# Kernel optimization log

Measured on AMD Instinct MI355X. Metric: run time of the kernel, lower is better.

The kernel has to match this reference:

```python
import jax, jax.numpy as jnp
import numpy as np

N, E = 100000, 1600000
IN_C, OUT_C, H, EDGE_DIM = 128, 64, 2, 4
NEG_SLOPE = 0.2
LN_EPS = 1e-5


def setup_inputs() -> dict:
    key = jax.random.key(0)
    ks = jax.random.split(key, 12)
    s = 1.0 / np.sqrt(IN_C)
    inp = {
        "x": jax.random.normal(ks[0], (N, IN_C), jnp.float32),
        "edge_index": jax.random.randint(ks[1], (2, E), 0, N, jnp.int64),
        "edge_attr": jax.random.normal(ks[2], (E, EDGE_DIM), jnp.float32),
        "W": jax.random.normal(ks[3], (IN_C, H * OUT_C), jnp.float32) * s,
        "att_src": jax.random.normal(ks[4], (H, OUT_C), jnp.float32) * s,
        "att_dst": jax.random.normal(ks[5], (H, OUT_C), jnp.float32) * s,
        "W_edge": jax.random.normal(ks[6], (EDGE_DIM, H * OUT_C), jnp.float32) * 0.5,
        "att_edge": jax.random.normal(ks[7], (H, OUT_C), jnp.float32) * s,
        "bias": jnp.zeros((OUT_C,), jnp.float32),
        "gamma": jnp.ones((OUT_C,), jnp.float32),
        "beta": jnp.zeros((OUT_C,), jnp.float32),
    }
    return inp


def reference(x, edge_index, edge_attr, W, att_src, att_dst, W_edge, att_edge, bias, gamma, beta):
    n = x.shape[0]
    src, dst = edge_index[0], edge_index[1]
    # shared src/dst linear (PyG GATConv with single input tensor)
    h = (x @ W).reshape(n, H, OUT_C)                       # [N,H,C]
    a_src = jnp.einsum("nhc,hc->nh", h, att_src)          # [N,H]
    a_dst = jnp.einsum("nhc,hc->nh", h, att_dst)          # [N,H]
    e = (edge_attr @ W_edge).reshape(-1, H, OUT_C)         # [E,H,C]
    a_edge = jnp.einsum("ehc,hc->eh", e, att_edge)        # [E,H]
    alpha = jax.nn.leaky_relu(a_src[src] + a_dst[dst] + a_edge, NEG_SLOPE)  # [E,H]
    # segment softmax over edges grouped by destination node
    amax = jax.ops.segment_max(alpha, dst, num_segments=n)
    ex = jnp.exp(alpha - amax[dst])
    denom = jax.ops.segment_sum(ex, dst, num_segments=n)
    w = ex / (denom[dst] + 1e-16)                          # [E,H]
    msg = h[src] * w[:, :, None]                           # [E,H,C]
    out = jax.ops.segment_sum(msg, dst, num_segments=n)    # [N,H,C]
    out = out.mean(axis=1) + bias                          # concat=False -> head mean
    # LayerNorm + ReLU
    mu = out.mean(-1, keepdims=True)
    var = ((out - mu) ** 2).mean(-1, keepdims=True)
    out = (out - mu) * jax.lax.rsqrt(var + LN_EPS) * gamma + beta
    return jax.nn.relu(out)
```

## Files before the change

kernel.cpp:

```cpp
#include <hip/hip_runtime.h>
#include <hip/hip_fp16.h>
#include <math.h>

#define IN_C 128
#define HC   128
#define OUT_C 64
#define NEG_SLOPE 0.2f
#define LN_EPS 1e-5f
#define CHUNK 4096
#define BSH   8
#define BMSK  255
#define NBMAX 512
#define NB2MAX 1024

typedef __attribute__((ext_vector_type(8))) _Float16 f16x8;
typedef __attribute__((ext_vector_type(4))) float f32x4;

__device__ inline unsigned h2pack(float a, float b) {
    __half2 h = __floats2half2_rn(a, b);
    return *reinterpret_cast<unsigned*>(&h);
}

__global__ __launch_bounds__(256) void k_pre(const float* __restrict__ W,
                                             const float* __restrict__ W_edge,
                                             const float* __restrict__ att_edge,
                                             const float* __restrict__ attS,
                                             const float* __restrict__ attD,
                                             const float* __restrict__ x,
                                             const int* __restrict__ ei_dst,
                                             unsigned short* __restrict__ WhT,
                                             float* __restrict__ V,
                                             int* __restrict__ off,
                                             float* __restrict__ a_src,
                                             float* __restrict__ a_dst,
                                             int E, int M, int NB, int PB) {
    __shared__ int hist[NBMAX];
    __shared__ float wsv0[128], wsv1[128], wdv0[128], wdv1[128];
    int b = blockIdx.x, t = threadIdx.x;
    if (b < 8) {
        #pragma unroll
        for (int i = 0; i < 8; ++i) {
            int idx = b * 2048 + i * 256 + t;
            int k = idx >> 7, col = idx & 127;
            __half hh = __float2half_rn(W[idx]);
            WhT[col * 128 + k] = *reinterpret_cast<unsigned short*>(&hh);
        }
        return;
    }
    if (b == 8) {
        if (t < 8) {
            int d = t >> 1, h = t & 1;
            float s = 0.f;
            for (int c = 0; c < 64; ++c)
                s += W_edge[d * HC + h * 64 + c] * att_edge[h * 64 + c];
            V[d * 2 + h] = s;
        }
        return;
    }
    int pb = b - 9;

    for (int i = t; i < NB; i += 256) hist[i] = 0;
    if (t < 128) {
        const float* wr = W + t * 128;
        float s0 = 0.f, s1 = 0.f, d0 = 0.f, d1 = 0.f;
        for (int c = 0; c < 64; ++c) {
            float w0 = wr[c], w1 = wr[64 + c];
            s0 += w0 * attS[c];      s1 += w1 * attS[64 + c];
            d0 += w0 * attD[c];      d1 += w1 * attD[64 + c];
        }
        wsv0[t] = s0; wsv1[t] = s1; wdv0[t] = d0; wdv1[t] = d1;
    }
    __syncthreads();

    if (pb < PB) {
        int base = pb * CHUNK;
        int lim = E - base; if (lim > CHUNK) lim = CHUNK;
        if (lim == CHUNK) {
            #pragma unroll
            for (int u = 0; u < 4; ++u) {
                int4 v = *(const int4*)&ei_dst[base + u * 1024 + t * 4];
                atomicAdd(&hist[v.x >> BSH], 1);
                atomicAdd(&hist[v.y >> BSH], 1);
                atomicAdd(&hist[v.z >> BSH], 1);
                atomicAdd(&hist[v.w >> BSH], 1);
            }
        } else {
            for (int i = t; i < lim; i += 256)
                atomicAdd(&hist[ei_dst[base + i] >> BSH], 1);
        }
    }
    {
        int n = pb * 256 + t;
        if (pb < NB && n < M) {
            const float4* xr4 = (const float4*)(x + (size_t)n * 128);
            float s0 = 0.f, s1 = 0.f, d0 = 0.f, d1 = 0.f;
            #pragma unroll 8
            for (int q = 0; q < 32; ++q) {
                float4 xv = xr4[q];
                int k = q * 4;
                s0 += xv.x * wsv0[k]     + xv.y * wsv0[k + 1]
                    + xv.z * wsv0[k + 2] + xv.w * wsv0[k + 3];
                s1 += xv.x * wsv1[k]     + xv.y * wsv1[k + 1]
                    + xv.z * wsv1[k + 2] + xv.w * wsv1[k + 3];
                d0 += xv.x * wdv0[k]     + xv.y * wdv0[k + 1]
                    + xv.z * wdv0[k + 2] + xv.w * wdv0[k + 3];
                d1 += xv.x * wdv1[k]     + xv.y * wdv1[k + 1]
                    + xv.z * wdv1[k + 2] + xv.w * wdv1[k + 3];
            }
            ((float2*)a_src)[n] = make_float2(s0, s1);
            ((float2*)a_dst)[n] = make_float2(d0, d1);
        }
    }
    __syncthreads();
    if (pb < PB)
        for (int i = t; i < NB; i += 256)
            off[(size_t)i * PB + pb] = hist[i];
}

__global__ __launch_bounds__(256) void k_scan(int* __restrict__ off,
                                              int* __restrict__ bsum, int nS) {
    __shared__ int sm[256];
    int t = threadIdx.x;
    int base = blockIdx.x * 1024 + t * 4;
    int v0 = 0, v1 = 0, v2 = 0, v3 = 0;
    if (base + 0 < nS) v0 = off[base + 0];
    if (base + 1 < nS) v1 = off[base + 1];
    if (base + 2 < nS) v2 = off[base + 2];
    if (base + 3 < nS) v3 = off[base + 3];
    int s = v0 + v1 + v2 + v3;
    sm[t] = s;
    __syncthreads();
    for (int o = 1; o < 256; o <<= 1) {
        int u = (t >= o) ? sm[t - o] : 0;
        __syncthreads();
        sm[t] += u;
        __syncthreads();
    }
    int excl = sm[t] - s;
    if (base + 0 < nS) off[base + 0] = excl;
    if (base + 1 < nS) off[base + 1] = excl + v0;
    if (base + 2 < nS) off[base + 2] = excl + v0 + v1;
    if (base + 3 < nS) off[base + 3] = excl + v0 + v1 + v2;
    if (t == 255) bsum[blockIdx.x] = sm[255];
}

__device__ inline void scan_bsum(const int* __restrict__ bsum, int nb2,
                                 int* bs, int* sm, int t) {
    int v0 = (4 * t + 0 < nb2) ? bsum[4 * t + 0] : 0;
    int v1 = (4 * t + 1 < nb2) ? bsum[4 * t + 1] : 0;
    int v2 = (4 * t + 2 < nb2) ? bsum[4 * t + 2] : 0;
    int v3 = (4 * t + 3 < nb2) ? bsum[4 * t + 3] : 0;
    int s = v0 + v1 + v2 + v3;
    sm[t] = s;
    __syncthreads();
    for (int o = 1; o < 256; o <<= 1) {
        int u = (t >= o) ? sm[t - o] : 0;
        __syncthreads();
        sm[t] += u;
        __syncthreads();
    }
    int excl = sm[t] - s;
    bs[4 * t + 0] = excl;
    bs[4 * t + 1] = excl + v0;
    bs[4 * t + 2] = excl + v0 + v1;
    bs[4 * t + 3] = excl + v0 + v1 + v2;
    __syncthreads();
}

__global__ __launch_bounds__(256) void k_fused(
        const float* __restrict__ x,
        const unsigned short* __restrict__ WhT,
        unsigned* __restrict__ hb, int M,
        const int* __restrict__ ei, const float* __restrict__ ea,
        const float* __restrict__ V,
        const float* __restrict__ a_src, const float* __restrict__ a_dst,
        const int* __restrict__ off, const int* __restrict__ bsum,
        int* __restrict__ bsum2, uint2* __restrict__ pA,
        int E, int NB, int PB, int nb2, int GB) {
    __shared__ unsigned xb[64 * 64];
    const int t = threadIdx.x;
    const int bid = blockIdx.x;
    const int r5 = bid % 5, g5 = bid / 5;

    if (r5 == 4) {
        int* cur = (int*)xb;
        int* bs  = (int*)xb + NBMAX;
        int* sm  = (int*)xb + NBMAX + NB2MAX;
        int pb = g5;
        scan_bsum(bsum, nb2, bs, sm, t);
        if (pb == 0)
            for (int i = t; i < nb2; i += 256) bsum2[i] = bs[i];
        for (int i = t; i < NB; i += 256) {
            size_t oi = (size_t)i * PB + pb;
            cur[i] = off[oi] + bs[(int)(oi >> 10)];
        }
        __syncthreads();
        float v0 = V[0], v1 = V[1], v2 = V[2], v3 = V[3];
        float v4 = V[4], v5 = V[5], v6 = V[6], v7 = V[7];
        int base = pb * CHUNK;
        int lim = E - base; if (lim > CHUNK) lim = CHUNK;
        if (lim == CHUNK) {
            #pragma unroll
            for (int h = 0; h < 2; ++h) {
                int e0 = base + h * 2048 + t;
                int sA[8], dA[8];
                #pragma unroll
                for (int k = 0; k < 8; ++k) {
                    sA[k] = ei[e0 + k * 256];
                    dA[k] = ei[E + e0 + k * 256];
                }
                float4 aA[8];
                #pragma unroll
                for (int k = 0; k < 8; ++k)
                    aA[k] = ((const float4*)ea)[e0 + k * 256];
                float2 asA[8], adA[8];
                #pragma unroll
                for (int k = 0; k < 8; ++k) {
                    asA[k] = ((const float2*)a_src)[sA[k]];
                    adA[k] = ((const float2*)a_dst)[dA[k]];
                }
                #pragma unroll
                for (int k = 0; k < 8; ++k) {
                    float ae0 = aA[k].x * v0 + aA[k].y * v2 + aA[k].z * v4 + aA[k].w * v6;
                    float ae1 = aA[k].x * v1 + aA[k].y * v3 + aA[k].z * v5 + aA[k].w * v7;
                    float al0 = asA[k].x + adA[k].x + ae0;
                    al0 = al0 > 0.f ? al0 : NEG_SLOPE * al0;
                    float al1 = asA[k].y + adA[k].y + ae1;
                    al1 = al1 > 0.f ? al1 : NEG_SLOPE * al1;
                    int slot = atomicAdd(&cur[dA[k] >> BSH], 1);
                    pA[slot] = make_uint2(
                        (unsigned)sA[k] | ((unsigned)(dA[k] & BMSK) << 17),
                        h2pack(__expf(al0), __expf(al1)));
                }
            }
        } else {
            for (int i = t; i < lim; i += 256) {
                int e = base + i;
                int s = ei[e], d = ei[E + e];
                float4 a = ((const float4*)ea)[e];
                float ae0 = a.x * v0 + a.y * v2 + a.z * v4 + a.w * v6;
                float ae1 = a.x * v1 + a.y * v3 + a.z * v5 + a.w * v7;
                float2 as = ((const float2*)a_src)[s];
                float2 ad = ((const float2*)a_dst)[d];
                float al0 = as.x + ad.x + ae0; al0 = al0 > 0.f ? al0 : NEG_SLOPE * al0;
                float al1 = as.y + ad.y + ae1; al1 = al1 > 0.f ? al1 : NEG_SLOPE * al1;
                int slot = atomicAdd(&cur[d >> BSH], 1);
                pA[slot] = make_uint2((unsigned)s | ((unsigned)(d & BMSK) << 17),
                                      h2pack(__expf(al0), __expf(al1)));
            }
        }
        return;
    }

    const int gid = g5 * 4 + r5;
    if (gid >= GB) return;
    const int brow = gid * 64;
    const float4* x4 = (const float4*)x;
    #pragma unroll
    for (int i = 0; i < 8; ++i) {
        int idx = i * 256 + t;
        int row = idx >> 5, c4 = idx & 31;
        float4 v = make_float4(0.f, 0.f, 0.f, 0.f);
        if (brow + row < M) v = x4[(size_t)(brow + row) * 32 + c4];
        unsigned lo = h2pack(v.x, v.y), hi = h2pack(v.z, v.w);
        int byte = row * 256 + ((c4 * 8) ^ ((row & 7) << 4));
        *(uint2*)((char*)xb + byte) = make_uint2(lo, hi);
    }
    __syncthreads();

    const int w = t >> 6, lane = t & 63;
    const int col = lane & 15, qr = lane >> 4;
    f32x4 acc[8];
    #pragma unroll
    for (int ct = 0; ct < 8; ++ct) acc[ct] = (f32x4){0.f, 0.f, 0.f, 0.f};

    const int arow = w * 16 + col;
    #pragma unroll
    for (int ks = 0; ks < 4; ++ks) {
        int abyte = arow * 256 + ((ks * 64 + qr * 16) ^ ((arow & 7) << 4));
        f16x8 af = *(const f16x8*)((const char*)xb + abyte);
        #pragma unroll
        for (int ct = 0; ct < 8; ++ct) {
            f16x8 bfr = *(const f16x8*)&WhT[(size_t)(ct * 16 + col) * 128 + ks * 32 + qr * 8];
            acc[ct] = __builtin_amdgcn_mfma_f32_16x16x32_f16(af, bfr, acc[ct], 0, 0, 0);
        }
    }

    #pragma unroll
    for (int r = 0; r < 4; ++r) {
        int grow = brow + w * 16 + qr * 4 + r;
        if (grow < M) {
            #pragma unroll
            for (int ct = 0; ct < 4; ++ct)
                hb[(size_t)grow * 64 + ct * 16 + col] =
                    h2pack(acc[ct][r], acc[ct + 4][r]);
        }
    }
}

__global__ __launch_bounds__(256) void k_csr(const uint2* __restrict__ pA,
                                             const int* __restrict__ off,
                                             const int* __restrict__ bsum2,
                                             int* __restrict__ rowptr,
                                             uint2* __restrict__ payload,
                                             int M, int E, int NB, int PB) {
    __shared__ int cnt[256];
    __shared__ int sc[256];
    __shared__ int cur[256];
    int b = blockIdx.x, t = threadIdx.x;
    int n0 = b << BSH;
    int nloc = M - n0; if (nloc > 256) nloc = 256;

    size_t o0 = (size_t)b * PB;
    int s0 = off[o0] + bsum2[(int)(o0 >> 10)];
    int s1 = E;
    if (b + 1 < NB) {
        size_t o1 = (size_t)(b + 1) * PB;
        s1 = off[o1] + bsum2[(int)(o1 >> 10)];
    }
    cnt[t] = 0;
    __syncthreads();

    for (int i = s0 + t; i < s1; i += 256)
        atomicAdd(&cnt[(pA[i].x >> 17) & BMSK], 1);
    __syncthreads();
    int c = cnt[t];
    sc[t] = c;
    __syncthreads();
    for (int o = 1; o < 256; o <<= 1) {
        int u = (t >= o) ? sc[t - o] : 0;
        __syncthreads();
        sc[t] += u;
        __syncthreads();
    }
    {
        int base = s0 + sc[t] - c;
        cur[t] = base;
        if (t < nloc) rowptr[n0 + t] = base;
    }
    if (b == NB - 1 && t == 0) rowptr[M] = E;
    __syncthreads();
    for (int i = s0 + t; i < s1; i += 256) {
        uint2 p = pA[i];
        int dl = (p.x >> 17) & BMSK;
        int pos = atomicAdd(&cur[dl], 1);
        payload[pos] = make_uint2(p.x & 0x1FFFF, p.y);
    }
}

__global__ __launch_bounds__(256) void k_gather(const uint2* __restrict__ payload,
                                                const int* __restrict__ rowptr,
                                                const unsigned* __restrict__ hb,
                                                const float* __restrict__ bias,
                                                const float* __restrict__ gamma,
                                                const float* __restrict__ beta,
                                                float* __restrict__ out, int M) {
    __shared__ uint2 stg[4][64];
    int w = threadIdx.x >> 6, lane = threadIdx.x & 63;
    int n = blockIdx.x * 4 + w;
    if (n >= M) return;
    int beg = rowptr[n], end = rowptr[n + 1];
    float acc0 = 0.f, acc1 = 0.f, pe0 = 0.f, pe1 = 0.f;

    for (int base = beg; base < end; base += 64) {
        int cnt = end - base; if (cnt > 64) cnt = 64;
        uint2 p = make_uint2(0u, 0u);
        if (lane < cnt) p = payload[base + lane];
        stg[w][lane] = p;
        {
            __half2 he = *reinterpret_cast<__half2*>(&p.y);
            pe0 += __low2float(he);
            pe1 += __high2float(he);
        }
        int j = 0;
        for (; j + 8 <= cnt; j += 8) {
            uint2 q0 = stg[w][j + 0], q1 = stg[w][j + 1];
            uint2 q2 = stg[w][j + 2], q3 = stg[w][j + 3];
            uint2 q4 = stg[w][j + 4], q5 = stg[w][j + 5];
            uint2 q6 = stg[w][j + 6], q7 = stg[w][j + 7];
            int s0 = __builtin_amdgcn_readfirstlane((int)q0.x);
            int s1 = __builtin_amdgcn_readfirstlane((int)q1.x);
            int s2 = __builtin_amdgcn_readfirstlane((int)q2.x);
            int s3 = __builtin_amdgcn_readfirstlane((int)q3.x);
            int s4 = __builtin_amdgcn_readfirstlane((int)q4.x);
            int s5 = __builtin_amdgcn_readfirstlane((int)q5.x);
            int s6 = __builtin_amdgcn_readfirstlane((int)q6.x);
            int s7 = __builtin_amdgcn_readfirstlane((int)q7.x);
            unsigned h0 = (hb + (size_t)s0 * 64)[lane];
            unsigned h1 = (hb + (size_t)s1 * 64)[lane];
            unsigned h2 = (hb + (size_t)s2 * 64)[lane];
            unsigned h3 = (hb + (size_t)s3 * 64)[lane];
            unsigned h4 = (hb + (size_t)s4 * 64)[lane];
            unsigned h5 = (hb + (size_t)s5 * 64)[lane];
            unsigned h6 = (hb + (size_t)s6 * 64)[lane];
            unsigned h7 = (hb + (size_t)s7 * 64)[lane];
            __half2 e0 = *reinterpret_cast<__half2*>(&q0.y);
            __half2 e1 = *reinterpret_cast<__half2*>(&q1.y);
            __half2 e2 = *reinterpret_cast<__half2*>(&q2.y);
            __half2 e3 = *reinterpret_cast<__half2*>(&q3.y);
            __half2 e4 = *reinterpret_cast<__half2*>(&q4.y);
            __half2 e5 = *reinterpret_cast<__half2*>(&q5.y);
            __half2 e6 = *reinterpret_cast<__half2*>(&q6.y);
            __half2 e7 = *reinterpret_cast<__half2*>(&q7.y);
            __half2 g0 = *reinterpret_cast<__half2*>(&h0);
            __half2 g1 = *reinterpret_cast<__half2*>(&h1);
            __half2 g2 = *reinterpret_cast<__half2*>(&h2);
            __half2 g3 = *reinterpret_cast<__half2*>(&h3);
            __half2 g4 = *reinterpret_cast<__half2*>(&h4);
            __half2 g5 = *reinterpret_cast<__half2*>(&h5);
            __half2 g6 = *reinterpret_cast<__half2*>(&h6);
            __half2 g7 = *reinterpret_cast<__half2*>(&h7);
            acc0 += __low2float(e0)  * __low2float(g0);
            acc1 += __high2float(e0) * __high2float(g0);
            acc0 += __low2float(e1)  * __low2float(g1);
            acc1 += __high2float(e1) * __high2float(g1);
            acc0 += __low2float(e2)  * __low2float(g2);
            acc1 += __high2float(e2) * __high2float(g2);
            acc0 += __low2float(e3)  * __low2float(g3);
            acc1 += __high2float(e3) * __high2float(g3);
            acc0 += __low2float(e4)  * __low2float(g4);
            acc1 += __high2float(e4) * __high2float(g4);
            acc0 += __low2float(e5)  * __low2float(g5);
            acc1 += __high2float(e5) * __high2float(g5);
            acc0 += __low2float(e6)  * __low2float(g6);
            acc1 += __high2float(e6) * __high2float(g6);
            acc0 += __low2float(e7)  * __low2float(g7);
            acc1 += __high2float(e7) * __high2float(g7);
        }
        for (; j + 4 <= cnt; j += 4) {
            uint2 q0 = stg[w][j + 0], q1 = stg[w][j + 1];
            uint2 q2 = stg[w][j + 2], q3 = stg[w][j + 3];
            int s0 = __builtin_amdgcn_readfirstlane((int)q0.x);
            int s1 = __builtin_amdgcn_readfirstlane((int)q1.x);
            int s2 = __builtin_amdgcn_readfirstlane((int)q2.x);
            int s3 = __builtin_amdgcn_readfirstlane((int)q3.x);
            unsigned h0 = (hb + (size_t)s0 * 64)[lane];
            unsigned h1 = (hb + (size_t)s1 * 64)[lane];
            unsigned h2 = (hb + (size_t)s2 * 64)[lane];
            unsigned h3 = (hb + (size_t)s3 * 64)[lane];
            __half2 e0 = *reinterpret_cast<__half2*>(&q0.y);
            __half2 e1 = *reinterpret_cast<__half2*>(&q1.y);
            __half2 e2 = *reinterpret_cast<__half2*>(&q2.y);
            __half2 e3 = *reinterpret_cast<__half2*>(&q3.y);
            __half2 g0 = *reinterpret_cast<__half2*>(&h0);
            __half2 g1 = *reinterpret_cast<__half2*>(&h1);
            __half2 g2 = *reinterpret_cast<__half2*>(&h2);
            __half2 g3 = *reinterpret_cast<__half2*>(&h3);
            acc0 += __low2float(e0)  * __low2float(g0);
            acc1 += __high2float(e0) * __high2float(g0);
            acc0 += __low2float(e1)  * __low2float(g1);
            acc1 += __high2float(e1) * __high2float(g1);
            acc0 += __low2float(e2)  * __low2float(g2);
            acc1 += __high2float(e2) * __high2float(g2);
            acc0 += __low2float(e3)  * __low2float(g3);
            acc1 += __high2float(e3) * __high2float(g3);
        }
        for (; j < cnt; ++j) {
            uint2 q0 = stg[w][j];
            int s0 = __builtin_amdgcn_readfirstlane((int)q0.x);
            unsigned h0 = (hb + (size_t)s0 * 64)[lane];
            __half2 e0 = *reinterpret_cast<__half2*>(&q0.y);
            __half2 g0 = *reinterpret_cast<__half2*>(&h0);
            acc0 += __low2float(e0)  * __low2float(g0);
            acc1 += __high2float(e0) * __high2float(g0);
        }
    }

    float d0 = pe0, d1 = pe1;
    #pragma unroll
    for (int m = 32; m; m >>= 1) {
        d0 += __shfl_xor(d0, m);
        d1 += __shfl_xor(d1, m);
    }

    float o = 0.5f * (acc0 / (d0 + 1e-16f) + acc1 / (d1 + 1e-16f)) + bias[lane];
    float mu = o;
    #pragma unroll
    for (int m = 32; m; m >>= 1) mu += __shfl_xor(mu, m);
    mu *= (1.f / 64.f);
    float c = o - mu;
    float v = c * c;
    #pragma unroll
    for (int m = 32; m; m >>= 1) v += __shfl_xor(v, m);
    v *= (1.f / 64.f);
    float y = c * rsqrtf(v + LN_EPS) * gamma[lane] + beta[lane];
    out[(size_t)n * OUT_C + lane] = fmaxf(y, 0.f);
}

extern "C" void kernel_launch(void* const* d_in, const int* in_sizes, int n_in,
                              void* d_out, int out_size, void* d_ws, size_t ws_size,
                              hipStream_t stream) {
    const float* x     = (const float*)d_in[0];
    const int*   ei    = (const int*)d_in[1];
    const float* ea    = (const float*)d_in[2];
    const float* W     = (const float*)d_in[3];
    const float* attS  = (const float*)d_in[4];
    const float* attD  = (const float*)d_in[5];
    const float* We    = (const float*)d_in[6];
    const float* attE  = (const float*)d_in[7];
    const float* bias  = (const float*)d_in[8];
    const float* gamma = (const float*)d_in[9];
    const float* beta  = (const float*)d_in[10];

    const int M  = in_sizes[0] / IN_C;
    const int E  = in_sizes[1] / 2;
    const int NB = (M + BMSK) >> BSH;
    const int PB = (E + CHUNK - 1) / CHUNK;
    const int nS = NB * PB;
    const int nb2 = (nS + 1023) / 1024;
    const int GB = (M + 63) / 64;
    const int PREB = (PB > NB ? PB : NB);

    char* ws = (char*)d_ws;
    size_t woff = 0;
    auto alloc = [&](size_t bytes) -> void* {
        void* p = ws + woff;
        woff += (bytes + 255) & ~(size_t)255;
        return p;
    };
    unsigned*       hb     = (unsigned*)      alloc((size_t)M * 64 * 4);
    float*          a_src  = (float*)         alloc((size_t)M * 2 * 4);
    float*          a_dst  = (float*)         alloc((size_t)M * 2 * 4);
    int*            off    = (int*)           alloc((size_t)nS * 4);
    int*            bsum   = (int*)           alloc((size_t)nb2 * 4);
    int*            bsum2  = (int*)           alloc((size_t)nb2 * 4);
    int*            rowptr = (int*)           alloc((size_t)(M + 1) * 4);
    uint2*          pA     = (uint2*)         alloc((size_t)E * 8);
    uint2*          payload= (uint2*)         alloc((size_t)E * 8);
    unsigned short* WhT    = (unsigned short*)alloc(128 * 128 * 2);
    float*          V      = (float*)         alloc(32);

    k_pre<<<9 + PREB, 256, 0, stream>>>(W, We, attE, attS, attD, x, ei + E,
                                        WhT, V, off, a_src, a_dst, E, M, NB, PB);
    k_scan<<<nb2, 256, 0, stream>>>(off, bsum, nS);
    k_fused<<<5 * PB, 256, 0, stream>>>(x, WhT, hb, M, ei, ea, V, a_src, a_dst,
                                        off, bsum, bsum2, pA, E, NB, PB, nb2, GB);
    k_csr<<<NB, 256, 0, stream>>>(pA, off, bsum2, rowptr, payload, M, E, NB, PB);
    k_gather<<<(M + 3) / 4, 256, 0, stream>>>(payload, rowptr, hb, bias, gamma, beta,
                                              (float*)d_out, M);
}
```

Measured before the change: 173.9 us.

## Defer attention logit and exp computation from partition pass to CSR pass

```diff
diff --git a/kernel.cpp b/kernel.cpp
--- a/kernel.cpp
+++ b/kernel.cpp
@@ -173,9 +173,9 @@
         unsigned* __restrict__ hb, int M,
         const int* __restrict__ ei, const float* __restrict__ ea,
         const float* __restrict__ V,
-        const float* __restrict__ a_src, const float* __restrict__ a_dst,
         const int* __restrict__ off, const int* __restrict__ bsum,
         int* __restrict__ bsum2, uint2* __restrict__ pA,
+        float* __restrict__ aeB,
         int E, int NB, int PB, int nb2, int GB) {
     __shared__ unsigned xb[64 * 64];
     const int t = threadIdx.x;
@@ -213,24 +213,15 @@
                 #pragma unroll
                 for (int k = 0; k < 8; ++k)
                     aA[k] = ((const float4*)ea)[e0 + k * 256];
-                float2 asA[8], adA[8];
-                #pragma unroll
-                for (int k = 0; k < 8; ++k) {
-                    asA[k] = ((const float2*)a_src)[sA[k]];
-                    adA[k] = ((const float2*)a_dst)[dA[k]];
-                }
                 #pragma unroll
                 for (int k = 0; k < 8; ++k) {
                     float ae0 = aA[k].x * v0 + aA[k].y * v2 + aA[k].z * v4 + aA[k].w * v6;
                     float ae1 = aA[k].x * v1 + aA[k].y * v3 + aA[k].z * v5 + aA[k].w * v7;
-                    float al0 = asA[k].x + adA[k].x + ae0;
-                    al0 = al0 > 0.f ? al0 : NEG_SLOPE * al0;
-                    float al1 = asA[k].y + adA[k].y + ae1;
-                    al1 = al1 > 0.f ? al1 : NEG_SLOPE * al1;
                     int slot = atomicAdd(&cur[dA[k] >> BSH], 1);
                     pA[slot] = make_uint2(
                         (unsigned)sA[k] | ((unsigned)(dA[k] & BMSK) << 17),
-                        h2pack(__expf(al0), __expf(al1)));
+                        __float_as_uint(ae0));
+                    aeB[slot] = ae1;
                 }
             }
         } else {
@@ -240,13 +231,10 @@
                 float4 a = ((const float4*)ea)[e];
                 float ae0 = a.x * v0 + a.y * v2 + a.z * v4 + a.w * v6;
                 float ae1 = a.x * v1 + a.y * v3 + a.z * v5 + a.w * v7;
-                float2 as = ((const float2*)a_src)[s];
-                float2 ad = ((const float2*)a_dst)[d];
-                float al0 = as.x + ad.x + ae0; al0 = al0 > 0.f ? al0 : NEG_SLOPE * al0;
-                float al1 = as.y + ad.y + ae1; al1 = al1 > 0.f ? al1 : NEG_SLOPE * al1;
                 int slot = atomicAdd(&cur[d >> BSH], 1);
                 pA[slot] = make_uint2((unsigned)s | ((unsigned)(d & BMSK) << 17),
-                                      h2pack(__expf(al0), __expf(al1)));
+                                      __float_as_uint(ae0));
+                aeB[slot] = ae1;
             }
         }
         return;
@@ -299,14 +287,18 @@
 }
 
 __global__ __launch_bounds__(256) void k_csr(const uint2* __restrict__ pA,
+                                             const float* __restrict__ aeB,
                                              const int* __restrict__ off,
                                              const int* __restrict__ bsum2,
+                                             const float* __restrict__ a_src,
+                                             const float* __restrict__ a_dst,
                                              int* __restrict__ rowptr,
                                              uint2* __restrict__ payload,
                                              int M, int E, int NB, int PB) {
     __shared__ int cnt[256];
     __shared__ int sc[256];
     __shared__ int cur[256];
+    __shared__ float2 adl[256];
     int b = blockIdx.x, t = threadIdx.x;
     int n0 = b << BSH;
     int nloc = M - n0; if (nloc > 256) nloc = 256;
@@ -319,6 +311,7 @@
         s1 = off[o1] + bsum2[(int)(o1 >> 10)];
     }
     cnt[t] = 0;
+    if (t < nloc) adl[t] = ((const float2*)a_dst)[n0 + t];
     __syncthreads();
 
     for (int i = s0 + t; i < s1; i += 256)
@@ -342,9 +335,17 @@
     __syncthreads();
     for (int i = s0 + t; i < s1; i += 256) {
         uint2 p = pA[i];
+        int src = p.x & 0x1FFFF;
         int dl = (p.x >> 17) & BMSK;
+        float ae0 = __uint_as_float(p.y);
+        float ae1 = aeB[i];
+        float2 as = ((const float2*)a_src)[src];
+        float2 ad = adl[dl];
+        float al0 = as.x + ad.x + ae0; al0 = al0 > 0.f ? al0 : NEG_SLOPE * al0;
+        float al1 = as.y + ad.y + ae1; al1 = al1 > 0.f ? al1 : NEG_SLOPE * al1;
         int pos = atomicAdd(&cur[dl], 1);
-        payload[pos] = make_uint2(p.x & 0x1FFFF, p.y);
+        payload[pos] = make_uint2((unsigned)src,
+                                  h2pack(__expf(al0), __expf(al1)));
     }
 }
 
@@ -526,6 +527,7 @@
     int*            bsum2  = (int*)           alloc((size_t)nb2 * 4);
     int*            rowptr = (int*)           alloc((size_t)(M + 1) * 4);
     uint2*          pA     = (uint2*)         alloc((size_t)E * 8);
+    float*          aeB    = (float*)         alloc((size_t)E * 4);
     uint2*          payload= (uint2*)         alloc((size_t)E * 8);
     unsigned short* WhT    = (unsigned short*)alloc(128 * 128 * 2);
     float*          V      = (float*)         alloc(32);
@@ -533,9 +535,11 @@
     k_pre<<<9 + PREB, 256, 0, stream>>>(W, We, attE, attS, attD, x, ei + E,
                                         WhT, V, off, a_src, a_dst, E, M, NB, PB);
     k_scan<<<nb2, 256, 0, stream>>>(off, bsum, nS);
-    k_fused<<<5 * PB, 256, 0, stream>>>(x, WhT, hb, M, ei, ea, V, a_src, a_dst,
-                                        off, bsum, bsum2, pA, E, NB, PB, nb2, GB);
-    k_csr<<<NB, 256, 0, stream>>>(pA, off, bsum2, rowptr, payload, M, E, NB, PB);
+    k_fused<<<5 * PB, 256, 0, stream>>>(x, WhT, hb, M, ei, ea, V,
+                                        off, bsum, bsum2, pA, aeB,
+                                        E, NB, PB, nb2, GB);
+    k_csr<<<NB, 256, 0, stream>>>(pA, aeB, off, bsum2, a_src, a_dst,
+                                  rowptr, payload, M, E, NB, PB);
     k_gather<<<(M + 3) / 4, 256, 0, stream>>>(payload, rowptr, hb, bias, gamma, beta,
                                               (float*)d_out, M);
 }
```

Result: faster. 169.0 us (median of 2 runs) (-2.8%).
